# Optimization experiments

Measured on AMD Instinct MI355X. Metric: run time of the kernel, lower is better.

## Reference

```python
import jax, jax.numpy as jnp
import numpy as np

EPS = 1e-5

def hardsigmoid(x):
    # torch F.hardsigmoid: clip(x/6 + 0.5, 0, 1)
    return jnp.clip(x / 6.0 + 0.5, 0.0, 1.0)

def setup_inputs() -> dict:
    T, B, D = 2048, 8, 1024
    key = jax.random.key(0)
    k1, k2 = jax.random.split(key)
    x = jax.random.normal(k1, (T, B, D), dtype=jnp.float32)
    c = jnp.zeros((B, D), dtype=jnp.float32)
    # params
    w_ufr = jax.random.normal(k2, (3 * D, D), dtype=jnp.float32) * (1.0 / np.sqrt(D))
    gamma = jnp.ones((D,), dtype=jnp.float32)
    beta = jnp.zeros((D,), dtype=jnp.float32)
    return {"x": x, "c": c, "w_ufr": w_ufr, "gamma": gamma, "beta": beta}

def reference(x, c, w_ufr, gamma, beta):
    residual = x
    # LayerNorm over last dim
    mu = jnp.mean(x, axis=-1, keepdims=True)
    var = jnp.mean(jnp.square(x - mu), axis=-1, keepdims=True)
    x_norm = (x - mu) * jax.lax.rsqrt(var + EPS) * gamma + beta
    # fused projection to u, f, r: (T,B,D) @ (D,3D)
    ufr = jnp.einsum('tbd,ed->tbe', x_norm, w_ufr)
    u, f, r = jnp.split(ufr, 3, axis=-1)
    f_gate = hardsigmoid(f)
    r_gate = hardsigmoid(r)
    # diagonal linear recurrence: c_t = f_t * c_{t-1} + (1 - f_t) * u_t
    def step(c_prev, inputs):
        ft, ut = inputs
        c_curr = ft * c_prev + (1.0 - ft) * ut
        return c_curr, c_curr
    c_last, c_all = jax.lax.scan(step, c, (f_gate, u))
    tanh_approx = c_all / (1.0 + jnp.abs(c_all))  # softsign
    hs = r_gate * tanh_approx + (1.0 - r_gate) * x_norm
    return (residual + hs, c_last)
```

## Files before the change

kernel.cpp:

```cpp
#include <hip/hip_runtime.h>
#include <stdint.h>


#define T_SEQ 2048
#define BATCH 8
#define DIM 1024
#define M_SZ (T_SEQ * BATCH)
#define N_SZ (3 * DIM)
#define K_SZ DIM
#define NCHUNK 32
#define CLEN (T_SEQ / NCHUNK)

#define GBM 256
#define GBN 256
#define GBK 32
#define NKT (K_SZ / GBK)

typedef __attribute__((ext_vector_type(8))) __bf16 bf16x8;
typedef __attribute__((ext_vector_type(4))) float f32x4;

__device__ __forceinline__ unsigned short f2bf(float f) {
  unsigned int u = __float_as_uint(f);
  u += 0x7FFFu + ((u >> 16) & 1u);
  return (unsigned short)(u >> 16);
}
__device__ __forceinline__ float bf2f(unsigned short s) {
  return __uint_as_float(((unsigned int)s) << 16);
}
__device__ __forceinline__ void gload16(const void* g, void* l) {
  __builtin_amdgcn_global_load_lds(
      (__attribute__((address_space(1))) void*)const_cast<void*>(g),
      (__attribute__((address_space(3))) void*)l, 16, 0, 0);
}

__global__ __launch_bounds__(256) void cvt_kernel(const float* __restrict__ w,
                                                  unsigned short* __restrict__ wb) {
  const int i = blockIdx.x * 256 + threadIdx.x;
  const float4 v = reinterpret_cast<const float4*>(w)[i];
  ushort4 o;
  o.x = f2bf(v.x); o.y = f2bf(v.y); o.z = f2bf(v.z); o.w = f2bf(v.w);
  reinterpret_cast<ushort4*>(wb)[i] = o;
}

__global__ __launch_bounds__(256) void ln_kernel(const float* __restrict__ x,
                                                 const float* __restrict__ gamma,
                                                 const float* __restrict__ beta,
                                                 unsigned short* __restrict__ xn) {
  const int row = blockIdx.x;
  const int tid = threadIdx.x;
  const float4 v = reinterpret_cast<const float4*>(x + (size_t)row * DIM)[tid];
  float s = v.x + v.y + v.z + v.w;
  float q = v.x * v.x + v.y * v.y + v.z * v.z + v.w * v.w;
#pragma unroll
  for (int off = 32; off > 0; off >>= 1) {
    s += __shfl_down(s, off);
    q += __shfl_down(q, off);
  }
  __shared__ float sbuf[8];
  const int wv = tid >> 6, ln = tid & 63;
  if (ln == 0) { sbuf[wv] = s; sbuf[4 + wv] = q; }
  __syncthreads();
  s = sbuf[0] + sbuf[1] + sbuf[2] + sbuf[3];
  q = sbuf[4] + sbuf[5] + sbuf[6] + sbuf[7];
  const float mu = s * (1.0f / DIM);
  const float rstd = rsqrtf(q * (1.0f / DIM) - mu * mu + 1e-5f);
  const float4 g = reinterpret_cast<const float4*>(gamma)[tid];
  const float4 b = reinterpret_cast<const float4*>(beta)[tid];
  ushort4 o;
  o.x = f2bf((v.x - mu) * rstd * g.x + b.x);
  o.y = f2bf((v.y - mu) * rstd * g.y + b.y);
  o.z = f2bf((v.z - mu) * rstd * g.z + b.z);
  o.w = f2bf((v.w - mu) * rstd * g.w + b.w);
  reinterpret_cast<ushort4*>(xn + (size_t)row * DIM)[tid] = o;
}

__global__ __launch_bounds__(512) void gemm_kernel(const unsigned short* __restrict__ A,
                                                   const unsigned short* __restrict__ W,
                                                   unsigned short* __restrict__ C) {
  __shared__ unsigned short smem[2 * 4 * GBM * GBK];
  const int tid = threadIdx.x;
  const int lane = tid & 63;
  const int wid = tid >> 6;
  const int wm = wid >> 2, wn = wid & 3;
  const int bm0 = blockIdx.y * GBM, bn0 = blockIdx.x * GBN;

  const int stgRow = wid * 32 + (lane >> 2);
  const int stgCol = ((lane & 3) ^ ((lane >> 3) & 3)) * 8;
  const unsigned short* gA = A + (size_t)(bm0 + stgRow) * K_SZ + stgCol;
  const unsigned short* gB = W + (size_t)(bn0 + stgRow) * K_SZ + stgCol;
  unsigned short* sAb = smem + wid * 32 * GBK;
  unsigned short* sBb = smem + 4 * GBM * GBK + wid * 32 * GBK;

#define STAGE(bufi, t) do {                                        \
    const size_t ko_ = (size_t)(t) * GBK;                          \
    unsigned short* sa_ = sAb + (bufi) * (GBM * GBK);              \
    unsigned short* sb_ = sBb + (bufi) * (GBN * GBK);              \
    gload16(gA + ko_, sa_);                                        \
    gload16(gA + ko_ + (size_t)16 * K_SZ, sa_ + 16 * GBK);         \
    gload16(gB + ko_, sb_);                                        \
    gload16(gB + ko_ + (size_t)16 * K_SZ, sb_ + 16 * GBK);         \
  } while (0)

  f32x4 acc[8][4] = {};
  const int fr = lane & 15;
  const int ko8 = ((lane >> 4) ^ ((fr >> 1) & 3)) * 8;

  STAGE(0, 0);
  STAGE(1, 1);
  STAGE(2, 2);
  asm volatile("s_waitcnt vmcnt(8)" ::: "memory");
  __builtin_amdgcn_s_barrier();
  asm volatile("" ::: "memory");

  for (int kt = 0; kt < NKT; ++kt) {
    const int cur = kt & 3;
    if (kt < NKT - 3) STAGE((kt + 3) & 3, kt + 3);

    const unsigned short* sa = smem + cur * (GBM * GBK);
    const unsigned short* sb = smem + 4 * GBM * GBK + cur * (GBN * GBK);
    bf16x8 af[8], bf[4];
#pragma unroll
    for (int i = 0; i < 8; i++)
      af[i] = *(const bf16x8*)&sa[(wm * 128 + i * 16 + fr) * GBK + ko8];
#pragma unroll
    for (int j = 0; j < 4; j++)
      bf[j] = *(const bf16x8*)&sb[(wn * 64 + j * 16 + fr) * GBK + ko8];

    __builtin_amdgcn_s_setprio(1);
#pragma unroll
    for (int i = 0; i < 8; i++)
#pragma unroll
      for (int j = 0; j < 4; j++)
        acc[i][j] = __builtin_amdgcn_mfma_f32_16x16x32_bf16(af[i], bf[j], acc[i][j], 0, 0, 0);
    __builtin_amdgcn_s_setprio(0);

    if (kt < NKT - 3)       asm volatile("s_waitcnt vmcnt(8)" ::: "memory");
    else if (kt == NKT - 3) asm volatile("s_waitcnt vmcnt(4)" ::: "memory");
    else if (kt == NKT - 2) asm volatile("s_waitcnt vmcnt(0)" ::: "memory");
    if (kt < NKT - 1) {
      __builtin_amdgcn_s_barrier();
      asm volatile("" ::: "memory");
    }
  }
#undef STAGE

  const int gate = (bn0 >= DIM);
  const int fq = lane >> 4;
#pragma unroll
  for (int i = 0; i < 8; i++) {
#pragma unroll
    for (int j = 0; j < 4; j++) {
      const int col = bn0 + wn * 64 + j * 16 + fr;
      size_t base = (size_t)(bm0 + wm * 128 + i * 16 + fq * 4) * N_SZ + col;
#pragma unroll
      for (int r = 0; r < 4; r++) {
        float v = acc[i][j][r];
        if (gate) v = fminf(fmaxf(v * (1.0f / 6.0f) + 0.5f, 0.0f), 1.0f);
        C[base + (size_t)r * N_SZ] = f2bf(v);
      }
    }
  }
}

__global__ __launch_bounds__(256) void scan1_kernel(const unsigned short* __restrict__ ufr,
                                                    float* __restrict__ Ac,
                                                    float* __restrict__ Bc) {
  const int lin = blockIdx.x * 256 + threadIdx.x;
  const int d = lin & (DIM - 1);
  const int b = (lin >> 10) & (BATCH - 1);
  const int g = lin >> 13;
  const unsigned short* p = ufr + (size_t)(g * CLEN) * (BATCH * N_SZ) + (size_t)b * N_SZ + d;
  float Aa = 1.0f, Bb = 0.0f;
#pragma unroll 8
  for (int t = 0; t < CLEN; t++) {
    const float u = bf2f(p[0]);
    const float f = bf2f(p[DIM]);
    Aa *= f;
    Bb = f * Bb + (1.0f - f) * u;
    p += BATCH * N_SZ;
  }
  Ac[lin] = Aa;
  Bc[lin] = Bb;
}

__global__ __launch_bounds__(256) void scan2_kernel(const float* __restrict__ Ac,
                                                    const float* __restrict__ Bc,
                                                    const float* __restrict__ c0,
                                                    float* __restrict__ cstart,
                                                    float* __restrict__ clast) {
  const int lin = blockIdx.x * 256 + threadIdx.x;
  float c = c0[lin];
#pragma unroll
  for (int g = 0; g < NCHUNK; g++) {
    cstart[g * (BATCH * DIM) + lin] = c;
    c = Ac[g * (BATCH * DIM) + lin] * c + Bc[g * (BATCH * DIM) + lin];
  }
  clast[lin] = c;
}

__global__ __launch_bounds__(256) void scan3_kernel(const unsigned short* __restrict__ ufr,
                                                    const unsigned short* __restrict__ xn,
                                                    const float* __restrict__ x,
                                                    const float* __restrict__ cstart,
                                                    float* __restrict__ out) {
  const int lin = blockIdx.x * 256 + threadIdx.x;
  const int d = lin & (DIM - 1);
  const int b = (lin >> 10) & (BATCH - 1);
  const int g = lin >> 13;
  float c = cstart[g * (BATCH * DIM) + b * DIM + d];
  const unsigned short* p = ufr + (size_t)(g * CLEN) * (BATCH * N_SZ) + (size_t)b * N_SZ + d;
  size_t xo = (size_t)(g * CLEN) * (BATCH * DIM) + (size_t)b * DIM + d;
#pragma unroll 4
  for (int t = 0; t < CLEN; t++) {
    const float u = bf2f(p[0]);
    const float f = bf2f(p[DIM]);
    const float r = bf2f(p[2 * DIM]);
    c = f * c + (1.0f - f) * u;
    const float ts = c / (1.0f + fabsf(c));
    const float xv = bf2f(xn[xo]);
    out[xo] = x[xo] + r * ts + (1.0f - r) * xv;
    p += BATCH * N_SZ;
    xo += BATCH * DIM;
  }
}

extern "C" void kernel_launch(void* const* d_in, const int* in_sizes, int n_in,
                              void* d_out, int out_size, void* d_ws, size_t ws_size,
                              hipStream_t stream) {
  const float* x = (const float*)d_in[0];
  const float* c0 = (const float*)d_in[1];
  const float* w = (const float*)d_in[2];
  const float* gamma = (const float*)d_in[3];
  const float* beta = (const float*)d_in[4];
  float* out = (float*)d_out;
  float* clast = out + (size_t)M_SZ * DIM;

  char* ws = (char*)d_ws;
  unsigned short* xn = (unsigned short*)ws;
  unsigned short* ufr = (unsigned short*)(ws + 33554432ull);
  float* Ac = (float*)(ws + 134217728ull);
  float* Bc = (float*)(ws + 135266304ull);
  float* cst = (float*)(ws + 136314880ull);
  unsigned short* wb = (unsigned short*)(ws + 137363456ull);

  cvt_kernel<<<(N_SZ * K_SZ / 4) / 256, 256, 0, stream>>>(w, wb);
  ln_kernel<<<M_SZ, 256, 0, stream>>>(x, gamma, beta, xn);
  dim3 ggrid(N_SZ / GBN, M_SZ / GBM);
  gemm_kernel<<<ggrid, 512, 0, stream>>>(xn, wb, ufr);
  scan1_kernel<<<(NCHUNK * BATCH * DIM) / 256, 256, 0, stream>>>(ufr, Ac, Bc);
  scan2_kernel<<<(BATCH * DIM) / 256, 256, 0, stream>>>(Ac, Bc, c0, cst, clast);
  scan3_kernel<<<(NCHUNK * BATCH * DIM) / 256, 256, 0, stream>>>(ufr, xn, x, cst, out);
}
```

Before: 206.8 us.

## Vectorize scan kernels, recompute LN in scan3, and remap GEMM blocks for XCD locality

The scan1 and scan3 kernels now handle four channels per thread, using 8-byte bf16 loads and 16-byte float loads and stores in place of scalar accesses. scan3 stops reading the bf16 normalized activations and instead recomputes them from x using per-row mean and rstd that the LayerNorm kernel now writes out. This removes one activation read, and the residual path now uses full fp32 normalized values. The GEMM grid becomes one-dimensional with a block-index remap that spreads tiles across the 8 chiplets. This is meant to improve L2 reuse but changes the tile execution order. The four-wide scans also cut the number of threads, which lowers parallelism in the latency-bound recurrence.

```diff
diff --git a/kernel.cpp b/kernel.cpp
--- a/kernel.cpp
+++ b/kernel.cpp
@@ -15,6 +15,8 @@
 #define GBN 256
 #define GBK 32
 #define NKT (K_SZ / GBK)
+#define NBX (N_SZ / GBN)
+#define NWG (NBX * (M_SZ / GBM))
 
 typedef __attribute__((ext_vector_type(8))) __bf16 bf16x8;
 typedef __attribute__((ext_vector_type(4))) float f32x4;
@@ -45,7 +47,9 @@
 __global__ __launch_bounds__(256) void ln_kernel(const float* __restrict__ x,
                                                  const float* __restrict__ gamma,
                                                  const float* __restrict__ beta,
-                                                 unsigned short* __restrict__ xn) {
+                                                 unsigned short* __restrict__ xn,
+                                                 float* __restrict__ muO,
+                                                 float* __restrict__ rsO) {
   const int row = blockIdx.x;
   const int tid = threadIdx.x;
   const float4 v = reinterpret_cast<const float4*>(x + (size_t)row * DIM)[tid];
@@ -64,6 +68,7 @@
   q = sbuf[4] + sbuf[5] + sbuf[6] + sbuf[7];
   const float mu = s * (1.0f / DIM);
   const float rstd = rsqrtf(q * (1.0f / DIM) - mu * mu + 1e-5f);
+  if (tid == 0) { muO[row] = mu; rsO[row] = rstd; }
   const float4 g = reinterpret_cast<const float4*>(gamma)[tid];
   const float4 b = reinterpret_cast<const float4*>(beta)[tid];
   ushort4 o;
@@ -82,7 +87,10 @@
   const int lane = tid & 63;
   const int wid = tid >> 6;
   const int wm = wid >> 2, wn = wid & 3;
-  const int bm0 = blockIdx.y * GBM, bn0 = blockIdx.x * GBN;
+
+  const int wg = (blockIdx.x & 7) * (NWG / 8) + (blockIdx.x >> 3);
+  const int bn0 = (wg % NBX) * GBN;
+  const int bm0 = (wg / NBX) * GBM;
 
   const int stgRow = wid * 32 + (lane >> 2);
   const int stgCol = ((lane & 3) ^ ((lane >> 3) & 3)) * 8;
@@ -94,7 +102,7 @@
 #define STAGE(bufi, t) do {                                        \
     const size_t ko_ = (size_t)(t) * GBK;                          \
     unsigned short* sa_ = sAb + (bufi) * (GBM * GBK);              \
-    unsigned short* sb_ = sBb + (bufi) * (GBN * GBK);              \
+    unsigned short* sb_ = sBb + (bufi) * (GBM * GBK);              \
     gload16(gA + ko_, sa_);                                        \
     gload16(gA + ko_ + (size_t)16 * K_SZ, sa_ + 16 * GBK);         \
     gload16(gB + ko_, sb_);                                        \
@@ -117,7 +125,7 @@
     if (kt < NKT - 3) STAGE((kt + 3) & 3, kt + 3);
 
     const unsigned short* sa = smem + cur * (GBM * GBK);
-    const unsigned short* sb = smem + 4 * GBM * GBK + cur * (GBN * GBK);
+    const unsigned short* sb = smem + 4 * GBM * GBK + cur * (GBM * GBK);
     bf16x8 af[8], bf[4];
 #pragma unroll
     for (int i = 0; i < 8; i++)
@@ -166,21 +174,27 @@
                                                     float* __restrict__ Ac,
                                                     float* __restrict__ Bc) {
   const int lin = blockIdx.x * 256 + threadIdx.x;
-  const int d = lin & (DIM - 1);
-  const int b = (lin >> 10) & (BATCH - 1);
-  const int g = lin >> 13;
-  const unsigned short* p = ufr + (size_t)(g * CLEN) * (BATCH * N_SZ) + (size_t)b * N_SZ + d;
-  float Aa = 1.0f, Bb = 0.0f;
-#pragma unroll 8
+  const int d0 = (lin & 255) << 2;
+  const int b = (lin >> 8) & (BATCH - 1);
+  const int g = lin >> 11;
+  const unsigned short* p = ufr + (size_t)(g * CLEN) * (BATCH * N_SZ) + (size_t)b * N_SZ + d0;
+  float Aa0 = 1.0f, Aa1 = 1.0f, Aa2 = 1.0f, Aa3 = 1.0f;
+  float Bb0 = 0.0f, Bb1 = 0.0f, Bb2 = 0.0f, Bb3 = 0.0f;
+#pragma unroll 4
   for (int t = 0; t < CLEN; t++) {
-    const float u = bf2f(p[0]);
-    const float f = bf2f(p[DIM]);
-    Aa *= f;
-    Bb = f * Bb + (1.0f - f) * u;
+    const ushort4 uu = *reinterpret_cast<const ushort4*>(p);
+    const ushort4 ff = *reinterpret_cast<const ushort4*>(p + DIM);
+    const float f0 = bf2f(ff.x), f1 = bf2f(ff.y), f2 = bf2f(ff.z), f3 = bf2f(ff.w);
+    Aa0 *= f0; Aa1 *= f1; Aa2 *= f2; Aa3 *= f3;
+    Bb0 = f0 * Bb0 + (1.0f - f0) * bf2f(uu.x);
+    Bb1 = f1 * Bb1 + (1.0f - f1) * bf2f(uu.y);
+    Bb2 = f2 * Bb2 + (1.0f - f2) * bf2f(uu.z);
+    Bb3 = f3 * Bb3 + (1.0f - f3) * bf2f(uu.w);
     p += BATCH * N_SZ;
   }
-  Ac[lin] = Aa;
-  Bc[lin] = Bb;
+  const int o = g * (BATCH * DIM) + b * DIM + d0;
+  *reinterpret_cast<float4*>(&Ac[o]) = make_float4(Aa0, Aa1, Aa2, Aa3);
+  *reinterpret_cast<float4*>(&Bc[o]) = make_float4(Bb0, Bb1, Bb2, Bb3);
 }
 
 __global__ __launch_bounds__(256) void scan2_kernel(const float* __restrict__ Ac,
@@ -199,28 +213,60 @@
 }
 
 __global__ __launch_bounds__(256) void scan3_kernel(const unsigned short* __restrict__ ufr,
-                                                    const unsigned short* __restrict__ xn,
                                                     const float* __restrict__ x,
                                                     const float* __restrict__ cstart,
+                                                    const float* __restrict__ muA,
+                                                    const float* __restrict__ rsA,
+                                                    const float* __restrict__ gamma,
+                                                    const float* __restrict__ beta,
                                                     float* __restrict__ out) {
   const int lin = blockIdx.x * 256 + threadIdx.x;
-  const int d = lin & (DIM - 1);
-  const int b = (lin >> 10) & (BATCH - 1);
-  const int g = lin >> 13;
-  float c = cstart[g * (BATCH * DIM) + b * DIM + d];
-  const unsigned short* p = ufr + (size_t)(g * CLEN) * (BATCH * N_SZ) + (size_t)b * N_SZ + d;
-  size_t xo = (size_t)(g * CLEN) * (BATCH * DIM) + (size_t)b * DIM + d;
-#pragma unroll 4
+  const int d0 = (lin & 255) << 2;
+  const int b = (lin >> 8) & (BATCH - 1);
+  const int g = lin >> 11;
+  const float4 cs = *reinterpret_cast<const float4*>(&cstart[g * (BATCH * DIM) + b * DIM + d0]);
+  float c0 = cs.x, c1 = cs.y, c2 = cs.z, c3 = cs.w;
+  const float4 gm = *reinterpret_cast<const float4*>(&gamma[d0]);
+  const float4 bt = *reinterpret_cast<const float4*>(&beta[d0]);
+  const unsigned short* p = ufr + (size_t)(g * CLEN) * (BATCH * N_SZ) + (size_t)b * N_SZ + d0;
+  size_t xo = (size_t)(g * CLEN) * (BATCH * DIM) + (size_t)b * DIM + d0;
+  int row = g * CLEN * BATCH + b;
+#pragma unroll 2
   for (int t = 0; t < CLEN; t++) {
-    const float u = bf2f(p[0]);
-    const float f = bf2f(p[DIM]);
-    const float r = bf2f(p[2 * DIM]);
-    c = f * c + (1.0f - f) * u;
-    const float ts = c / (1.0f + fabsf(c));
-    const float xv = bf2f(xn[xo]);
-    out[xo] = x[xo] + r * ts + (1.0f - r) * xv;
+    const ushort4 uu = *reinterpret_cast<const ushort4*>(p);
+    const ushort4 ff = *reinterpret_cast<const ushort4*>(p + DIM);
+    const ushort4 rr = *reinterpret_cast<const ushort4*>(p + 2 * DIM);
+    const float4 xv = *reinterpret_cast<const float4*>(&x[xo]);
+    const float mu = muA[row], rs = rsA[row];
+    float o[4];
+    {
+      const float f = bf2f(ff.x), r = bf2f(rr.x);
+      const float xnv = (xv.x - mu) * rs * gm.x + bt.x;
+      c0 = f * c0 + (1.0f - f) * bf2f(uu.x);
+      o[0] = xv.x + r * (c0 / (1.0f + fabsf(c0))) + (1.0f - r) * xnv;
+    }
+    {
+      const float f = bf2f(ff.y), r = bf2f(rr.y);
+      const float xnv = (xv.y - mu) * rs * gm.y + bt.y;
+      c1 = f * c1 + (1.0f - f) * bf2f(uu.y);
+      o[1] = xv.y + r * (c1 / (1.0f + fabsf(c1))) + (1.0f - r) * xnv;
+    }
+    {
+      const float f = bf2f(ff.z), r = bf2f(rr.z);
+      const float xnv = (xv.z - mu) * rs * gm.z + bt.z;
+      c2 = f * c2 + (1.0f - f) * bf2f(uu.z);
+      o[2] = xv.z + r * (c2 / (1.0f + fabsf(c2))) + (1.0f - r) * xnv;
+    }
+    {
+      const float f = bf2f(ff.w), r = bf2f(rr.w);
+      const float xnv = (xv.w - mu) * rs * gm.w + bt.w;
+      c3 = f * c3 + (1.0f - f) * bf2f(uu.w);
+      o[3] = xv.w + r * (c3 / (1.0f + fabsf(c3))) + (1.0f - r) * xnv;
+    }
+    *reinterpret_cast<float4*>(&out[xo]) = make_float4(o[0], o[1], o[2], o[3]);
     p += BATCH * N_SZ;
     xo += BATCH * DIM;
+    row += BATCH;
   }
 }
 
@@ -242,12 +288,14 @@
   float* Bc = (float*)(ws + 135266304ull);
   float* cst = (float*)(ws + 136314880ull);
   unsigned short* wb = (unsigned short*)(ws + 137363456ull);
+  float* muA = (float*)(ws + 143654912ull);
+  float* rsA = (float*)(ws + 143720448ull);
 
   cvt_kernel<<<(N_SZ * K_SZ / 4) / 256, 256, 0, stream>>>(w, wb);
-  ln_kernel<<<M_SZ, 256, 0, stream>>>(x, gamma, beta, xn);
-  dim3 ggrid(N_SZ / GBN, M_SZ / GBM);
-  gemm_kernel<<<ggrid, 512, 0, stream>>>(xn, wb, ufr);
-  scan1_kernel<<<(NCHUNK * BATCH * DIM) / 256, 256, 0, stream>>>(ufr, Ac, Bc);
+  ln_kernel<<<M_SZ, 256, 0, stream>>>(x, gamma, beta, xn, muA, rsA);
+  gemm_kernel<<<NWG, 512, 0, stream>>>(xn, wb, ufr);
+  scan1_kernel<<<(NCHUNK * BATCH * DIM / 4) / 256, 256, 0, stream>>>(ufr, Ac, Bc);
   scan2_kernel<<<(BATCH * DIM) / 256, 256, 0, stream>>>(Ac, Bc, c0, cst, clast);
-  scan3_kernel<<<(NCHUNK * BATCH * DIM) / 256, 256, 0, stream>>>(ufr, xn, x, cst, out);
-}
+  scan3_kernel<<<(NCHUNK * BATCH * DIM / 4) / 256, 256, 0, stream>>>(
+      ufr, x, cst, muA, rsA, gamma, beta, out);
+}
```

After: 199.3 us. -3.7%, faster.
